# Kernel tuning notes

Measured on AMD Instinct MI355X. Metric: run time of the kernel, lower is better.

The kernel has to match this reference:

```python
import jax, jax.numpy as jnp
import numpy as np
import math

B = 8; T = 340; M = 32; H = 512; NH = 8; DH = H // NH; NB = 4; NA = 4
OBS = 64; MAXT = 1000
INFO = 3 * T; L = INFO + 2 * M  # 1084


def build_mask():
    # Replicates: causal tril over info tokens, then F.pad((0,M,M,0),0) and F.pad((M,0,0,M),1):
    # read-token columns (first M) visible to everyone; write-token rows (last M) attend to all;
    # read-token rows see only read tokens; info tokens are causal over info tokens.
    core = jnp.tril(jnp.ones((INFO, INFO), jnp.float32))
    m = jnp.zeros((L, L), jnp.float32)
    m = m.at[M:M + INFO, M:M + INFO].set(core)
    m = m.at[:, :M].set(1.0)
    m = m.at[-M:, :].set(1.0)
    return m


def layer_norm(x, g, b, eps=1e-5):
    mu = x.mean(-1, keepdims=True)
    var = ((x - mu) ** 2).mean(-1, keepdims=True)
    return (x - mu) / jnp.sqrt(var + eps) * g + b


def setup_inputs() -> dict:
    key = jax.random.key(0)
    ks = jax.random.split(key, 24)
    def n(k, shape, s=0.02):
        return jax.random.normal(k, shape, jnp.float32) * s
    return {
        "returns": jax.random.normal(ks[0], (B, T, 1), jnp.float32),
        "actions": jax.random.normal(ks[1], (B, T, 1), jnp.float32),
        "t_table": n(ks[2], (MAXT, H)),
        "s_table": n(ks[3], (OBS, H)),
        "Wr": n(ks[4], (H, 1)), "br": jnp.zeros((H,), jnp.float32),
        "Wa": n(ks[5], (H, 1)), "ba": jnp.zeros((H,), jnp.float32),
        "ln_e_g": jnp.ones((H,), jnp.float32), "ln_e_b": jnp.zeros((H,), jnp.float32),
        "read_mem": n(ks[6], (M, H)), "mem_tok": n(ks[7], (M, H)),
        "Wq": n(ks[8], (NB, H, H)), "bq": jnp.zeros((NB, H), jnp.float32),
        "Wk": n(ks[9], (NB, H, H)), "bk": jnp.zeros((NB, H), jnp.float32),
        "Wv": n(ks[10], (NB, H, H)), "bv": jnp.zeros((NB, H), jnp.float32),
        "Wo": n(ks[11], (NB, H, H)), "bo": jnp.zeros((NB, H), jnp.float32),
        "W1": n(ks[12], (NB, 4 * H, H)), "b1": jnp.zeros((NB, 4 * H), jnp.float32),
        "W2": n(ks[13], (NB, H, 4 * H)), "b2": jnp.zeros((NB, H), jnp.float32),
        "g1": jnp.ones((NB, H), jnp.float32), "be1": jnp.zeros((NB, H), jnp.float32),
        "g2": jnp.ones((NB, H), jnp.float32), "be2": jnp.zeros((NB, H), jnp.float32),
        "Wp": n(ks[14], (NA, H)), "bp": jnp.zeros((NA,), jnp.float32),
        "states": jax.random.randint(ks[15], (B, T), 0, OBS),
        "timestep": jax.random.randint(ks[16], (B, T), 0, MAXT),
    }


def _forward(returns, actions, t_table, s_table, Wr, br, Wa, ba, ln_e_g, ln_e_b,
             read_mem, mem_tok, Wq, bq, Wk, bk, Wv, bv, Wo, bo,
             W1, b1, W2, b2, g1, be1, g2, be2, Wp, bp, states, timestep):
    mask = build_mask()  # (L, L)
    te = t_table[timestep]                      # (B,T,H)
    re = returns @ Wr.T + br + te               # (B,T,H)
    se = s_table[states]                        # (B,T,H)
    ae = actions @ Wa.T + ba + te               # (B,T,H)
    hidden = jnp.stack([re, se, ae], axis=2).reshape(B, INFO, H)  # interleave r,s,a
    hidden = jnp.concatenate([
        jnp.broadcast_to(read_mem, (B, M, H)),
        hidden,
        jnp.broadcast_to(mem_tok, (B, M, H)),
    ], axis=1)                                  # (B,L,H)
    hidden = layer_norm(hidden, ln_e_g, ln_e_b)

    scale = 1.0 / math.sqrt(DH)

    def block(x, p):
        wq, bq_, wk, bk_, wv, bv_, wo, bo_, w1, b1_, w2, b2_, gg1, bb1, gg2, bb2 = p
        q = (x @ wq.T + bq_).reshape(B, L, NH, DH).transpose(0, 2, 1, 3)
        k = (x @ wk.T + bk_).reshape(B, L, NH, DH).transpose(0, 2, 1, 3)
        v = (x @ wv.T + bv_).reshape(B, L, NH, DH).transpose(0, 2, 1, 3)
        w = jnp.einsum('bnid,bnjd->bnij', q, k) * scale  # (B,NH,L,L)
        w = jnp.where(mask == 0, -jnp.inf, w)
        a = jax.nn.softmax(w, axis=-1)
        o = jnp.einsum('bnij,bnjd->bnid', a, v).transpose(0, 2, 1, 3).reshape(B, L, H)
        x = x + (o @ wo.T + bo_)
        x = layer_norm(x, gg1, bb1)
        m = jax.nn.gelu(x @ w1.T + b1_, approximate=False) @ w2.T + b2_
        x = layer_norm(x + m, gg2, bb2)
        return x, None

    hidden, _ = jax.lax.scan(
        block, hidden,
        (Wq, bq, Wk, bk, Wv, bv, Wo, bo, W1, b1, W2, b2, g1, be1, g2, be2))

    memory_output = hidden[:, -M:, :]
    core = hidden[:, M:-M, :].reshape(B, T, 3, H)
    action_logits = core[:, :, 1] @ Wp.T + bp   # predict from state-token hiddens
    return action_logits, memory_output


def reference(returns, actions, t_table, s_table, Wr, br, Wa, ba, ln_e_g, ln_e_b,
              read_mem, mem_tok, Wq, bq, Wk, bk, Wv, bv, Wo, bo,
              W1, b1, W2, b2, g1, be1, g2, be2, Wp, bp, states, timestep):
    return _forward(returns, actions, t_table, s_table, Wr, br, Wa, ba, ln_e_g, ln_e_b,
                    read_mem, mem_tok, Wq, bq, Wk, bk, Wv, bv, Wo, bo,
                    W1, b1, W2, b2, g1, be1, g2, be2, Wp, bp, states, timestep)
```

## Files before the change

### kernel.cpp

```cpp
#include <hip/hip_runtime.h>
#include <hip/hip_bf16.h>

typedef unsigned short ushort_t;
typedef __attribute__((ext_vector_type(8))) __bf16 bf16x8;
typedef __attribute__((ext_vector_type(4))) float f32x4;
typedef __attribute__((ext_vector_type(16))) float f32x16;
typedef __attribute__((ext_vector_type(2))) unsigned u32x2;
typedef __attribute__((ext_vector_type(4))) unsigned u32x4;

#define B_ 8
#define T_ 340
#define M_ 32
#define H_ 512
#define NH_ 8
#define DH_ 64
#define INFO_ 1020
#define L_ 1084
#define LP_ 1088
#define MROWS 8672
#define MPAD 8704
#define HMLP 2048

__device__ __forceinline__ ushort_t f2bf(float f) {
  unsigned u = __builtin_bit_cast(unsigned, f);
  unsigned r = (u + 0x7fffu + ((u >> 16) & 1u)) >> 16;
  return (ushort_t)r;
}

__device__ __forceinline__ float bflo(unsigned u) {
  return __builtin_bit_cast(float, u << 16);
}
__device__ __forceinline__ float bfhi(unsigned u) {
  return __builtin_bit_cast(float, u & 0xffff0000u);
}

__device__ __forceinline__ unsigned cvtpk_bf16(float lo, float hi) {
  unsigned r;
  asm volatile("v_cvt_pk_bf16_f32 %0, %1, %2" : "=v"(r) : "v"(lo), "v"(hi));
  return r;
}

__device__ __forceinline__ void gload16(const ushort_t* g, ushort_t* l) {
  __builtin_amdgcn_global_load_lds((const __attribute__((address_space(1))) unsigned*)g,
                                   (__attribute__((address_space(3))) unsigned*)l, 16, 0, 0);
}

__global__ __launch_bounds__(256) void zero_pads_kernel(ushort_t* Qb, ushort_t* Kb,
                                                        ushort_t* Vt, ushort_t* Ob) {
  int idx = blockIdx.x * 256 + threadIdx.x;
  if (idx < 16384) {
    int bh = idx >> 8;
    int rest = idx & 255;
    int l = L_ + (rest >> 6);
    int d = rest & 63;
    size_t o = ((size_t)bh * LP_ + l) * DH_ + d;
    Qb[o] = 0;
    Kb[o] = 0;
    Vt[((size_t)bh * DH_ + d) * LP_ + l] = 0;
  } else if (idx < 32768) {
    int j = idx - 16384;
    Ob[(size_t)MROWS * H_ + j] = 0;
  }
}

__global__ __launch_bounds__(256) void cvt8_kernel(const float* __restrict__ src,
                                                   ushort_t* __restrict__ dst, int n8) {
  int i = blockIdx.x * 256 + threadIdx.x;
  if (i >= n8) return;
  f32x4 a = ((const f32x4*)src)[2 * i];
  f32x4 b = ((const f32x4*)src)[2 * i + 1];
  u32x4 o;
  o.x = cvtpk_bf16(a[0], a[1]);
  o.y = cvtpk_bf16(a[2], a[3]);
  o.z = cvtpk_bf16(b[0], b[1]);
  o.w = cvtpk_bf16(b[2], b[3]);
  ((u32x4*)dst)[i] = o;
}

__global__ __launch_bounds__(256) void cvtqkv_kernel(const float* __restrict__ q,
                                                     const float* __restrict__ k,
                                                     const float* __restrict__ v,
                                                     ushort_t* __restrict__ dst) {
  int i8 = blockIdx.x * 256 + threadIdx.x;
  if (i8 >= 131072) return;
  int i = i8 * 8;
  int nb = i >> 18;
  int rem = i & 262143;
  size_t base8 = ((size_t)nb * 786432 + rem) >> 3;
  const float* srcs[3] = {q, k, v};
#pragma unroll
  for (int w = 0; w < 3; w++) {
    f32x4 a = ((const f32x4*)srcs[w])[2 * i8];
    f32x4 b = ((const f32x4*)srcs[w])[2 * i8 + 1];
    u32x4 o;
    o.x = cvtpk_bf16(a[0], a[1]);
    o.y = cvtpk_bf16(a[2], a[3]);
    o.z = cvtpk_bf16(b[0], b[1]);
    o.w = cvtpk_bf16(b[2], b[3]);
    ((u32x4*)dst)[base8 + (size_t)w * 32768] = o;
  }
}

__global__ __launch_bounds__(256) void biascat_kernel(const float* __restrict__ bq,
                                                      const float* __restrict__ bk,
                                                      const float* __restrict__ bv,
                                                      float* __restrict__ dst) {
  int i = blockIdx.x * 256 + threadIdx.x;
  if (i < 2048) {
    int nb = i >> 9, r = i & 511;
    float* d = dst + nb * 1536;
    d[r] = bq[i];
    d[512 + r] = bk[i];
    d[1024 + r] = bv[i];
  }
}

__global__ __launch_bounds__(256) void embed_ln_kernel(
    const float* __restrict__ returns, const float* __restrict__ actions,
    const float* __restrict__ t_table, const float* __restrict__ s_table,
    const float* __restrict__ Wr, const float* __restrict__ br,
    const float* __restrict__ Wa, const float* __restrict__ ba,
    const float* __restrict__ g, const float* __restrict__ be,
    const float* __restrict__ read_mem, const float* __restrict__ mem_tok,
    const int* __restrict__ states, const int* __restrict__ timestep,
    ushort_t* __restrict__ Xb) {
  const int row = blockIdx.x;
  const int tid = threadIdx.x;
  if (row >= MROWS) {
    Xb[(size_t)row * H_ + tid] = 0;
    Xb[(size_t)row * H_ + tid + 256] = 0;
    return;
  }
  const int b = row / L_, l = row - b * L_;
  float v[2];
#pragma unroll
  for (int s2 = 0; s2 < 2; s2++) {
    int hh = tid + s2 * 256;
    float val;
    if (l < M_) {
      val = read_mem[(size_t)l * H_ + hh];
    } else if (l >= M_ + INFO_) {
      val = mem_tok[(size_t)(l - M_ - INFO_) * H_ + hh];
    } else {
      int ii = l - M_;
      int t = ii / 3, c = ii - t * 3;
      int bt = b * T_ + t;
      if (c == 1) {
        val = s_table[(size_t)states[bt] * H_ + hh];
      } else {
        float te = t_table[(size_t)timestep[bt] * H_ + hh];
        val = (c == 0 ? returns[bt] * Wr[hh] + br[hh] : actions[bt] * Wa[hh] + ba[hh]) + te;
      }
    }
    v[s2] = val;
  }
  float sum = v[0] + v[1], sq = v[0] * v[0] + v[1] * v[1];
  __shared__ float sa[4], sb[4];
#pragma unroll
  for (int o = 1; o < 64; o <<= 1) {
    sum += __shfl_xor(sum, o);
    sq += __shfl_xor(sq, o);
  }
  int wv = tid >> 6, lane = tid & 63;
  if (lane == 0) { sa[wv] = sum; sb[wv] = sq; }
  __syncthreads();
  sum = sa[0] + sa[1] + sa[2] + sa[3];
  sq = sb[0] + sb[1] + sb[2] + sb[3];
  float mu = sum * (1.0f / H_);
  float var = sq * (1.0f / H_) - mu * mu;
  float rstd = rsqrtf(var + 1e-5f);
#pragma unroll
  for (int s2 = 0; s2 < 2; s2++) {
    int hh = tid + s2 * 256;
    float y = (v[s2] - mu) * rstd * g[hh] + be[hh];
    Xb[(size_t)row * H_ + hh] = f2bf(y);
  }
}

__global__ __launch_bounds__(256) void ln_add_kernel(ushort_t* __restrict__ Xb,
                                                     const ushort_t* __restrict__ Y,
                                                     const float* __restrict__ g,
                                                     const float* __restrict__ be) {
  const int row = blockIdx.x;
  const int tid = threadIdx.x;
  unsigned* xr = (unsigned*)(Xb + (size_t)row * H_);
  if (row >= MROWS) {
    xr[tid] = 0;
    return;
  }
  const unsigned* yr = (const unsigned*)(Y + (size_t)row * H_);
  unsigned xu = xr[tid], yu = yr[tid];
  float v0 = bflo(xu) + bflo(yu);
  float v1 = bfhi(xu) + bfhi(yu);
  float sum = v0 + v1, sq = v0 * v0 + v1 * v1;
  __shared__ float sa[4], sb[4];
#pragma unroll
  for (int o = 1; o < 64; o <<= 1) {
    sum += __shfl_xor(sum, o);
    sq += __shfl_xor(sq, o);
  }
  int wv = tid >> 6, lane = tid & 63;
  if (lane == 0) { sa[wv] = sum; sb[wv] = sq; }
  __syncthreads();
  sum = sa[0] + sa[1] + sa[2] + sa[3];
  sq = sb[0] + sb[1] + sb[2] + sb[3];
  float mu = sum * (1.0f / H_);
  float var = sq * (1.0f / H_) - mu * mu;
  float rstd = rsqrtf(var + 1e-5f);
  float g0 = g[2 * tid], g1v = g[2 * tid + 1];
  float b0 = be[2 * tid], b1v = be[2 * tid + 1];
  float n0 = (v0 - mu) * rstd * g0 + b0;
  float n1 = (v1 - mu) * rstd * g1v + b1v;
  xr[tid] = cvtpk_bf16(n0, n1);
}

template <int MODE>
__global__ __launch_bounds__(256, 3) void gemm_kernel(const ushort_t* __restrict__ A,
                                                      const ushort_t* __restrict__ W,
                                                      const float* __restrict__ bias,
                                                      void* __restrict__ o0,
                                                      void* __restrict__ o1,
                                                      void* __restrict__ o2, int Ntiles,
                                                      int K) {
  __shared__ ushort_t As[2][8192];
  __shared__ ushort_t Bs[2][4096];
  const int tid = threadIdx.x;
  const int job = (blockIdx.x & 7) * (gridDim.x >> 3) + (blockIdx.x >> 3);
  const int bx = job % Ntiles, by = job / Ntiles;
  const int m0 = by * 128, n0 = bx * 64;
  const int lane = tid & 63, wv = tid >> 6;
  const int wr = wv >> 1, wc = wv & 1;
  f32x4 acc[4][2] = {};

  const int srow = lane >> 3;
  const int kg = (lane & 7) ^ srow;
  const ushort_t* Asrc[4];
  const ushort_t* Bsrc[2];
#pragma unroll
  for (int g2 = 0; g2 < 4; g2++) {
    int row = wv * 32 + g2 * 8 + srow;
    Asrc[g2] = A + (size_t)(m0 + row) * K + kg * 8;
  }
#pragma unroll
  for (int g2 = 0; g2 < 2; g2++) {
    int row = wv * 16 + g2 * 8 + srow;
    Bsrc[g2] = W + (size_t)(n0 + row) * K + kg * 8;
  }
  ushort_t* ldsA[2] = {&As[0][wv * 2048], &As[1][wv * 2048]};
  ushort_t* ldsB[2] = {&Bs[0][wv * 1024], &Bs[1][wv * 1024]};

  const int NT = K >> 6;

#pragma unroll
  for (int g2 = 0; g2 < 4; g2++) gload16(Asrc[g2], ldsA[0] + g2 * 512);
#pragma unroll
  for (int g2 = 0; g2 < 2; g2++) gload16(Bsrc[g2], ldsB[0] + g2 * 512);

  const int q = lane >> 4, lr = lane & 15;
  const int s0 = q ^ (lr & 7);
  const int s1 = (4 + q) ^ (lr & 7);

  auto compute_tile = [&](int cur) {
    bf16x8 af[4][2], bfr[2][2];
#pragma unroll
    for (int mi = 0; mi < 4; mi++) {
      const ushort_t* rp = &As[cur][(wr * 64 + mi * 16 + lr) * 64];
      af[mi][0] = *(const bf16x8*)(rp + s0 * 8);
      af[mi][1] = *(const bf16x8*)(rp + s1 * 8);
    }
#pragma unroll
    for (int ni = 0; ni < 2; ni++) {
      const ushort_t* rp = &Bs[cur][(wc * 32 + ni * 16 + lr) * 64];
      bfr[ni][0] = *(const bf16x8*)(rp + s0 * 8);
      bfr[ni][1] = *(const bf16x8*)(rp + s1 * 8);
    }
#pragma unroll
    for (int kc = 0; kc < 2; kc++)
#pragma unroll
      for (int mi = 0; mi < 4; mi++)
#pragma unroll
        for (int ni = 0; ni < 2; ni++)
          acc[mi][ni] =
              __builtin_amdgcn_mfma_f32_16x16x32_bf16(af[mi][kc], bfr[ni][kc], acc[mi][ni], 0, 0, 0);
  };

  for (int kt = 0; kt < NT - 1; kt++) {
    const int cur = kt & 1, nxt = cur ^ 1;
    const int k0n = (kt + 1) << 6;
#pragma unroll
    for (int g2 = 0; g2 < 4; g2++) gload16(Asrc[g2] + k0n, ldsA[nxt] + g2 * 512);
#pragma unroll
    for (int g2 = 0; g2 < 2; g2++) gload16(Bsrc[g2] + k0n, ldsB[nxt] + g2 * 512);
    asm volatile("s_waitcnt vmcnt(6)" ::: "memory");
    __builtin_amdgcn_s_barrier();
    asm volatile("" ::: "memory");
    compute_tile(cur);
    asm volatile("" ::: "memory");
    __builtin_amdgcn_s_barrier();
  }
  {
    asm volatile("s_waitcnt vmcnt(0)" ::: "memory");
    __builtin_amdgcn_s_barrier();
    asm volatile("" ::: "memory");
    compute_tile((NT - 1) & 1);
  }

#pragma unroll
  for (int mi = 0; mi < 4; mi++) {
    const int mbase = m0 + wr * 64 + mi * 16 + ((lane >> 4) << 2);
    const bool mok = mbase < MROWS;
    int bb = 0, lbase = 0;
    if (MODE == 0) {
      bb = mbase / L_;
      lbase = mbase - bb * L_;
    }
#pragma unroll
    for (int ni = 0; ni < 2; ni++) {
      const int n = n0 + wc * 32 + ni * 16 + (lane & 15);
      float v[4];
#pragma unroll
      for (int r = 0; r < 4; r++) v[r] = acc[mi][ni][r] + bias[n];
      if (MODE == 0) {
        if (mok) {
          const int which = n >> 9, nn = n & 511;
          const int hh = nn >> 6, d = nn & 63;
          if (which == 0) {
            ushort_t* o = (ushort_t*)o0 + (((size_t)(bb * NH_ + hh)) * LP_ + lbase) * DH_ + d;
#pragma unroll
            for (int r = 0; r < 4; r++)
              o[(size_t)r * DH_] = f2bf(v[r] * 0.18033688011112043f);
          } else if (which == 1) {
            ushort_t* o = (ushort_t*)o1 + (((size_t)(bb * NH_ + hh)) * LP_ + lbase) * DH_ + d;
#pragma unroll
            for (int r = 0; r < 4; r++) o[(size_t)r * DH_] = f2bf(v[r]);
          } else {
            u32x2 w2;
            w2.x = cvtpk_bf16(v[0], v[1]);
            w2.y = cvtpk_bf16(v[2], v[3]);
            *(u32x2*)((ushort_t*)o2 + (((size_t)(bb * NH_ + hh)) * DH_ + d) * LP_ + lbase) = w2;
          }
        }
      } else if (MODE == 2) {
        if (mok) {
#pragma unroll
          for (int r = 0; r < 4; r++)
            ((ushort_t*)o0)[(size_t)(mbase + r) * H_ + n] = f2bf(v[r]);
        }
      } else {
#pragma unroll
        for (int r = 0; r < 4; r++) {
          float ge = 0.5f * v[r] * (1.0f + erff(v[r] * 0.70710678f));
          ((ushort_t*)o0)[(size_t)(mbase + r) * HMLP + n] = f2bf(ge);
        }
      }
    }
  }
}

__global__ __launch_bounds__(256, 3) void attn_kernel(const ushort_t* __restrict__ Qb,
                                                      const ushort_t* __restrict__ Kb,
                                                      const ushort_t* __restrict__ Vt,
                                                      ushort_t* __restrict__ Ob) {
  __shared__ ushort_t Klds[2][2048];
  __shared__ ushort_t Vlds[2][2048];
  const int tid = threadIdx.x;
  const int lane = tid & 63, wv = tid >> 6;
  const int xcd = blockIdx.x & 7, slot = blockIdx.x >> 3;
  const int g = slot >> 3, bhi = slot & 7;
  const int bh = (bhi << 3) | xcd;
  const int t = 33 - 4 * g - wv;
  const bool active = (t >= 0);
  const int b = bh >> 3, h = bh & 7;
  const int qb = t * 32;
  const int lq = lane & 31, hi = lane >> 5;
  const int nk_own = active ? ((t == 33) ? 34 : (t + 1)) : 0;
  const int nkmax = (g == 0) ? 34 : (34 - 4 * g);
  const int cmask = (t == 0) ? -1 : (nk_own - 1);
  const int i = qb + lq;

  const ushort_t* Qp = Qb + (size_t)bh * LP_ * DH_;
  const ushort_t* Kp = Kb + (size_t)bh * LP_ * DH_;
  const ushort_t* Vp = Vt + (size_t)bh * DH_ * LP_;

  const ushort_t* KsrcB =
      Kp + (size_t)(8 * wv + (lane >> 3)) * DH_ + (((lane & 7) ^ ((lane >> 3) & 7)) * 8);
  const ushort_t* VsrcB =
      Vp + (size_t)(16 * wv + (lane >> 2)) * LP_ + (((lane & 3) ^ ((lane >> 3) & 3)) * 8);
  ushort_t* KdstA = &Klds[0][wv * 512];
  ushort_t* KdstB = &Klds[1][wv * 512];
  ushort_t* VdstA = &Vlds[0][wv * 512];
  ushort_t* VdstB = &Vlds[1][wv * 512];

  bf16x8 qf[4];
  if (active) {
#pragma unroll
    for (int dc = 0; dc < 4; dc++)
      qf[dc] = *(const bf16x8*)(Qp + (size_t)(qb + lq) * DH_ + dc * 16 + hi * 8);
  }
  asm volatile("s_waitcnt vmcnt(0)" ::: "memory");

  f32x16 o0 = {}, o1 = {};
  float lsum = 0.f;

  int koff[4], voff[4];
#pragma unroll
  for (int dc = 0; dc < 4; dc++) koff[dc] = lq * 64 + (((dc * 2 + hi) ^ (lq & 7)) * 8);
#pragma unroll
  for (int f = 0; f < 4; f++) {
    int dt = f >> 1, cc = f & 1;
    voff[f] = (dt * 32 + lq) * 32 + ((((cc * 2 + hi) ^ ((lq >> 1) & 3))) * 8);
  }

  gload16(KsrcB, KdstA);
  gload16(VsrcB, VdstA);

  for (int c = 0; c < nkmax; c++) {
    const int cur = c & 1;
    const bool more = (c + 1 < nkmax);
    if (more) {
      const ushort_t* ks = KsrcB + (size_t)(c + 1) * 2048;
      const ushort_t* vs = VsrcB + (c + 1) * 32;
      if (cur) {
        gload16(ks, KdstA);
        gload16(vs, VdstA);
      } else {
        gload16(ks, KdstB);
        gload16(vs, VdstB);
      }
      asm volatile("s_waitcnt vmcnt(2)" ::: "memory");
    } else {
      asm volatile("s_waitcnt vmcnt(0)" ::: "memory");
    }
    __builtin_amdgcn_s_barrier();
    asm volatile("" ::: "memory");

    if (c < nk_own) {
      bf16x8 kf[4], vf[4];
#pragma unroll
      for (int dc = 0; dc < 4; dc++) kf[dc] = *(const bf16x8*)&Klds[cur][koff[dc]];
#pragma unroll
      for (int f = 0; f < 4; f++) vf[f] = *(const bf16x8*)&Vlds[cur][voff[f]];

      f32x16 s = {};
#pragma unroll
      for (int dc = 0; dc < 4; dc++)
        s = __builtin_amdgcn_mfma_f32_32x32x16_bf16(kf[dc], qf[dc], s, 0, 0, 0);
      float p[16];
      if (c == cmask) {
#pragma unroll
        for (int r = 0; r < 16; r++) {
          int jcol = c * 32 + (r & 3) + 8 * (r >> 2) + 4 * hi;
          bool ok = (jcol < L_) && ((jcol < M_) || (i >= M_ + INFO_) || (jcol <= i));
          p[r] = ok ? __builtin_amdgcn_exp2f(s[r]) : 0.f;
        }
      } else {
#pragma unroll
        for (int r = 0; r < 16; r++) p[r] = __builtin_amdgcn_exp2f(s[r]);
      }
      float u0 = (p[0] + p[1]) + (p[2] + p[3]);
      float u1 = (p[4] + p[5]) + (p[6] + p[7]);
      float u2 = (p[8] + p[9]) + (p[10] + p[11]);
      float u3 = (p[12] + p[13]) + (p[14] + p[15]);
      lsum += (u0 + u1) + (u2 + u3);
      bf16x8 pf[2];
#pragma unroll
      for (int cc = 0; cc < 2; cc++) {
        unsigned A01 = cvtpk_bf16(p[8 * cc + 0], p[8 * cc + 1]);
        unsigned A23 = cvtpk_bf16(p[8 * cc + 2], p[8 * cc + 3]);
        unsigned B45 = cvtpk_bf16(p[8 * cc + 4], p[8 * cc + 5]);
        unsigned B67 = cvtpk_bf16(p[8 * cc + 6], p[8 * cc + 7]);
        u32x2 r0 = __builtin_amdgcn_permlane32_swap(A01, B45, false, false);
        u32x2 r1 = __builtin_amdgcn_permlane32_swap(A23, B67, false, false);
        u32x4 w = {r0.x, r1.x, r0.y, r1.y};
        pf[cc] = __builtin_bit_cast(bf16x8, w);
      }
      o0 = __builtin_amdgcn_mfma_f32_32x32x16_bf16(vf[0], pf[0], o0, 0, 0, 0);
      o0 = __builtin_amdgcn_mfma_f32_32x32x16_bf16(vf[1], pf[1], o0, 0, 0, 0);
      o1 = __builtin_amdgcn_mfma_f32_32x32x16_bf16(vf[2], pf[0], o1, 0, 0, 0);
      o1 = __builtin_amdgcn_mfma_f32_32x32x16_bf16(vf[3], pf[1], o1, 0, 0, 0);
    }
    asm volatile("" ::: "memory");
    __builtin_amdgcn_s_barrier();
  }

  if (active) {
    u32x2 tt = __builtin_amdgcn_permlane32_swap(__builtin_bit_cast(unsigned, lsum),
                                                __builtin_bit_cast(unsigned, lsum), false, false);
    lsum = __builtin_bit_cast(float, tt.x) + __builtin_bit_cast(float, tt.y);
    if (i < L_) {
      const float inv = 1.0f / lsum;
      ushort_t* orow = Ob + ((size_t)(b * L_ + i)) * H_ + h * DH_;
#pragma unroll
      for (int dt = 0; dt < 2; dt++) {
#pragma unroll
        for (int q2 = 0; q2 < 4; q2++) {
          float v0 = (dt ? o1[4 * q2 + 0] : o0[4 * q2 + 0]) * inv;
          float v1 = (dt ? o1[4 * q2 + 1] : o0[4 * q2 + 1]) * inv;
          float v2 = (dt ? o1[4 * q2 + 2] : o0[4 * q2 + 2]) * inv;
          float v3 = (dt ? o1[4 * q2 + 3] : o0[4 * q2 + 3]) * inv;
          int dbase = dt * 32 + 8 * q2 + 4 * hi;
          *(unsigned*)(orow + dbase) = cvtpk_bf16(v0, v1);
          *(unsigned*)(orow + dbase + 2) = cvtpk_bf16(v2, v3);
        }
      }
    }
  }
}

__global__ __launch_bounds__(64) void logits_kernel(const ushort_t* __restrict__ Xb,
                                                    const float* __restrict__ Wp,
                                                    const float* __restrict__ bp,
                                                    float* __restrict__ out) {
  const int bt = blockIdx.x;
  const int b = bt / T_, t = bt - b * T_;
  const int lane = threadIdx.x;
  const ushort_t* xr = Xb + ((size_t)(b * L_ + M_ + 3 * t + 1)) * H_ + lane * 8;
  u32x4 xv = *(const u32x4*)xr;
  float x0[8];
#pragma unroll
  for (int ii = 0; ii < 4; ii++) {
    unsigned u = xv[ii];
    x0[2 * ii] = bflo(u);
    x0[2 * ii + 1] = bfhi(u);
  }
#pragma unroll
  for (int a = 0; a < 4; a++) {
    const float* wr2 = Wp + (size_t)a * H_ + lane * 8;
    float p = 0.f;
#pragma unroll
    for (int ii = 0; ii < 8; ii++) p += x0[ii] * wr2[ii];
#pragma unroll
    for (int o = 1; o < 64; o <<= 1) p += __shfl_xor(p, o);
    if (lane == 0) out[(size_t)bt * 4 + a] = p + bp[a];
  }
}

__global__ __launch_bounds__(256) void memout_kernel(const ushort_t* __restrict__ Xb,
                                                     float* __restrict__ out) {
  int idx = blockIdx.x * 256 + threadIdx.x;
  if (idx < B_ * M_ * H_ / 2) {
    int e = idx * 2;
    int b = e >> 14;
    int rest = e & 16383;
    int r = rest >> 9;
    int hh = rest & 511;
    unsigned u = *(const unsigned*)&Xb[((size_t)(b * L_ + M_ + INFO_ + r)) * H_ + hh];
    out[e] = bflo(u);
    out[e + 1] = bfhi(u);
  }
}

extern "C" void kernel_launch(void* const* d_in, const int* in_sizes, int n_in, void* d_out,
                              int out_size, void* d_ws, size_t ws_size, hipStream_t stream) {
  const float* returns = (const float*)d_in[0];
  const float* actions = (const float*)d_in[1];
  const float* t_table = (const float*)d_in[2];
  const float* s_table = (const float*)d_in[3];
  const float* Wr = (const float*)d_in[4];
  const float* br = (const float*)d_in[5];
  const float* Wa = (const float*)d_in[6];
  const float* ba = (const float*)d_in[7];
  const float* ln_e_g = (const float*)d_in[8];
  const float* ln_e_b = (const float*)d_in[9];
  const float* read_mem = (const float*)d_in[10];
  const float* mem_tok = (const float*)d_in[11];
  const float* Wq = (const float*)d_in[12];
  const float* bq = (const float*)d_in[13];
  const float* Wk = (const float*)d_in[14];
  const float* bk = (const float*)d_in[15];
  const float* Wv = (const float*)d_in[16];
  const float* bv = (const float*)d_in[17];
  const float* Wo = (const float*)d_in[18];
  const float* bo = (const float*)d_in[19];
  const float* W1 = (const float*)d_in[20];
  const float* b1 = (const float*)d_in[21];
  const float* W2 = (const float*)d_in[22];
  const float* b2 = (const float*)d_in[23];
  const float* g1 = (const float*)d_in[24];
  const float* be1 = (const float*)d_in[25];
  const float* g2 = (const float*)d_in[26];
  const float* be2 = (const float*)d_in[27];
  const float* Wp = (const float*)d_in[28];
  const float* bp = (const float*)d_in[29];
  const int* states = (const int*)d_in[30];
  const int* timestep = (const int*)d_in[31];

  char* ws = (char*)d_ws;
  size_t off = 0;
  auto alloc = [&](size_t bytes) -> char* {
    char* p = ws + off;
    off += (bytes + 255) & ~(size_t)255;
    return p;
  };
  ushort_t* Xb = (ushort_t*)alloc((size_t)MPAD * H_ * 2);
  ushort_t* Y = (ushort_t*)alloc((size_t)MPAD * H_ * 2);
  ushort_t* Qb = (ushort_t*)alloc((size_t)B_ * NH_ * LP_ * DH_ * 2);
  ushort_t* Kb2 = (ushort_t*)alloc((size_t)B_ * NH_ * LP_ * DH_ * 2);
  ushort_t* Vt = (ushort_t*)alloc((size_t)B_ * NH_ * DH_ * LP_ * 2);
  ushort_t* Ob = (ushort_t*)alloc((size_t)MPAD * H_ * 2);
  ushort_t* Hm = (ushort_t*)alloc((size_t)MPAD * HMLP * 2);
  ushort_t* Wqkvb = (ushort_t*)alloc((size_t)4 * 1536 * 512 * 2);
  ushort_t* Wob = (ushort_t*)alloc((size_t)4 * 512 * 512 * 2);
  ushort_t* W1b = (ushort_t*)alloc((size_t)4 * 2048 * 512 * 2);
  ushort_t* W2b = (ushort_t*)alloc((size_t)4 * 512 * 2048 * 2);
  float* biascat = (float*)alloc((size_t)4 * 1536 * 4);

  zero_pads_kernel<<<128, 256, 0, stream>>>(Qb, Kb2, Vt, Ob);
  cvtqkv_kernel<<<512, 256, 0, stream>>>(Wq, Wk, Wv, Wqkvb);
  biascat_kernel<<<8, 256, 0, stream>>>(bq, bk, bv, biascat);
  cvt8_kernel<<<512, 256, 0, stream>>>(Wo, Wob, 4 * 512 * 512 / 8);
  cvt8_kernel<<<2048, 256, 0, stream>>>(W1, W1b, 4 * 2048 * 512 / 8);
  cvt8_kernel<<<2048, 256, 0, stream>>>(W2, W2b, 4 * 512 * 2048 / 8);

  embed_ln_kernel<<<MPAD, 256, 0, stream>>>(returns, actions, t_table, s_table, Wr, br, Wa,
                                            ba, ln_e_g, ln_e_b, read_mem, mem_tok, states,
                                            timestep, Xb);

  for (int nb = 0; nb < 4; ++nb) {
    const size_t wo512 = (size_t)nb * 512 * 512;
    const size_t woqkv = (size_t)nb * 1536 * 512;
    const size_t wo1 = (size_t)nb * 2048 * 512;
    gemm_kernel<0><<<68 * 24, 256, 0, stream>>>(Xb, Wqkvb + woqkv, biascat + nb * 1536, Qb,
                                                Kb2, Vt, 24, 512);
    attn_kernel<<<576, 256, 0, stream>>>(Qb, Kb2, Vt, Ob);
    gemm_kernel<2><<<68 * 8, 256, 0, stream>>>(Ob, Wob + wo512, bo + nb * 512, Y, nullptr,
                                               nullptr, 8, 512);
    ln_add_kernel<<<MPAD, 256, 0, stream>>>(Xb, Y, g1 + nb * 512, be1 + nb * 512);
    gemm_kernel<3><<<68 * 32, 256, 0, stream>>>(Xb, W1b + wo1, b1 + nb * 2048, Hm, nullptr,
                                                nullptr, 32, 512);
    gemm_kernel<2><<<68 * 8, 256, 0, stream>>>(Hm, W2b + wo1, b2 + nb * 512, Y, nullptr,
                                               nullptr, 8, 2048);
    ln_add_kernel<<<MPAD, 256, 0, stream>>>(Xb, Y, g2 + nb * 512, be2 + nb * 512);
  }

  logits_kernel<<<B_ * T_, 64, 0, stream>>>(Xb, Wp, bp, (float*)d_out);
  memout_kernel<<<256, 256, 0, stream>>>(Xb, (float*)d_out + (size_t)B_ * T_ * 4);
}
```

Measured before the change: 627.0 us.

## Triple-buffer LDS prefetch in GEMM and attention kernels

Both the GEMM and attention kernels move from double to triple buffering, issuing global-to-LDS loads two tiles ahead and adjusting vmcnt waits to match. The aim is to hide more global memory latency behind MFMA compute. In exchange the GEMM's LDS use grows from 48KB to 72KB and its launch bound drops from 3 to 2 blocks per CU, lowering occupancy. The attention kernel also drops the wait on the Q loads, so that wait now folds into the first loop iteration's vmcnt.

New measurement: 804.3 us. +28.3%, slower.

```diff
diff --git a/kernel.cpp b/kernel.cpp
--- a/kernel.cpp
+++ b/kernel.cpp
@@ -215,15 +215,15 @@
 }
 
 template <int MODE>
-__global__ __launch_bounds__(256, 3) void gemm_kernel(const ushort_t* __restrict__ A,
+__global__ __launch_bounds__(256, 2) void gemm_kernel(const ushort_t* __restrict__ A,
                                                       const ushort_t* __restrict__ W,
                                                       const float* __restrict__ bias,
                                                       void* __restrict__ o0,
                                                       void* __restrict__ o1,
                                                       void* __restrict__ o2, int Ntiles,
                                                       int K) {
-  __shared__ ushort_t As[2][8192];
-  __shared__ ushort_t Bs[2][4096];
+  __shared__ ushort_t As[3][8192];
+  __shared__ ushort_t Bs[3][4096];
   const int tid = threadIdx.x;
   const int job = (blockIdx.x & 7) * (gridDim.x >> 3) + (blockIdx.x >> 3);
   const int bx = job % Ntiles, by = job / Ntiles;
@@ -246,15 +246,21 @@
     int row = wv * 16 + g2 * 8 + srow;
     Bsrc[g2] = W + (size_t)(n0 + row) * K + kg * 8;
   }
-  ushort_t* ldsA[2] = {&As[0][wv * 2048], &As[1][wv * 2048]};
-  ushort_t* ldsB[2] = {&Bs[0][wv * 1024], &Bs[1][wv * 1024]};
 
   const int NT = K >> 6;
 
-#pragma unroll
-  for (int g2 = 0; g2 < 4; g2++) gload16(Asrc[g2], ldsA[0] + g2 * 512);
-#pragma unroll
-  for (int g2 = 0; g2 < 2; g2++) gload16(Bsrc[g2], ldsB[0] + g2 * 512);
+  auto stage = [&](int kt, int buf) {
+    const int k0 = kt << 6;
+    ushort_t* la = &As[buf][wv * 2048];
+    ushort_t* lb = &Bs[buf][wv * 1024];
+#pragma unroll
+    for (int g2 = 0; g2 < 4; g2++) gload16(Asrc[g2] + k0, la + g2 * 512);
+#pragma unroll
+    for (int g2 = 0; g2 < 2; g2++) gload16(Bsrc[g2] + k0, lb + g2 * 512);
+  };
+
+  stage(0, 0);
+  if (NT > 1) stage(1, 1);
 
   const int q = lane >> 4, lr = lane & 15;
   const int s0 = q ^ (lr & 7);
@@ -284,25 +290,21 @@
               __builtin_amdgcn_mfma_f32_16x16x32_bf16(af[mi][kc], bfr[ni][kc], acc[mi][ni], 0, 0, 0);
   };
 
-  for (int kt = 0; kt < NT - 1; kt++) {
-    const int cur = kt & 1, nxt = cur ^ 1;
-    const int k0n = (kt + 1) << 6;
-#pragma unroll
-    for (int g2 = 0; g2 < 4; g2++) gload16(Asrc[g2] + k0n, ldsA[nxt] + g2 * 512);
-#pragma unroll
-    for (int g2 = 0; g2 < 2; g2++) gload16(Bsrc[g2] + k0n, ldsB[nxt] + g2 * 512);
-    asm volatile("s_waitcnt vmcnt(6)" ::: "memory");
+  for (int kt = 0; kt < NT; kt++) {
+    const int nxt2 = kt + 2;
+    if (nxt2 < NT) stage(nxt2, nxt2 % 3);
+    if (nxt2 < NT) {
+      asm volatile("s_waitcnt vmcnt(12)" ::: "memory");
+    } else if (kt + 1 < NT) {
+      asm volatile("s_waitcnt vmcnt(6)" ::: "memory");
+    } else {
+      asm volatile("s_waitcnt vmcnt(0)" ::: "memory");
+    }
     __builtin_amdgcn_s_barrier();
     asm volatile("" ::: "memory");
-    compute_tile(cur);
+    compute_tile(kt % 3);
     asm volatile("" ::: "memory");
     __builtin_amdgcn_s_barrier();
-  }
-  {
-    asm volatile("s_waitcnt vmcnt(0)" ::: "memory");
-    __builtin_amdgcn_s_barrier();
-    asm volatile("" ::: "memory");
-    compute_tile((NT - 1) & 1);
   }
 
 #pragma unroll
@@ -361,8 +363,8 @@
                                                       const ushort_t* __restrict__ Kb,
                                                       const ushort_t* __restrict__ Vt,
                                                       ushort_t* __restrict__ Ob) {
-  __shared__ ushort_t Klds[2][2048];
-  __shared__ ushort_t Vlds[2][2048];
+  __shared__ ushort_t Klds[3][2048];
+  __shared__ ushort_t Vlds[3][2048];
   const int tid = threadIdx.x;
   const int lane = tid & 63, wv = tid >> 6;
   const int xcd = blockIdx.x & 7, slot = blockIdx.x >> 3;
@@ -386,10 +388,14 @@
       Kp + (size_t)(8 * wv + (lane >> 3)) * DH_ + (((lane & 7) ^ ((lane >> 3) & 7)) * 8);
   const ushort_t* VsrcB =
       Vp + (size_t)(16 * wv + (lane >> 2)) * LP_ + (((lane & 3) ^ ((lane >> 3) & 3)) * 8);
-  ushort_t* KdstA = &Klds[0][wv * 512];
-  ushort_t* KdstB = &Klds[1][wv * 512];
-  ushort_t* VdstA = &Vlds[0][wv * 512];
-  ushort_t* VdstB = &Vlds[1][wv * 512];
+
+  auto stageKV = [&](int c, int buf) {
+    gload16(KsrcB + (size_t)c * 2048, &Klds[buf][wv * 512]);
+    gload16(VsrcB + c * 32, &Vlds[buf][wv * 512]);
+  };
+
+  stageKV(0, 0);
+  if (nkmax > 1) stageKV(1, 1);
 
   bf16x8 qf[4];
   if (active) {
@@ -397,7 +403,6 @@
     for (int dc = 0; dc < 4; dc++)
       qf[dc] = *(const bf16x8*)(Qp + (size_t)(qb + lq) * DH_ + dc * 16 + hi * 8);
   }
-  asm volatile("s_waitcnt vmcnt(0)" ::: "memory");
 
   f32x16 o0 = {}, o1 = {};
   float lsum = 0.f;
@@ -411,22 +416,13 @@
     voff[f] = (dt * 32 + lq) * 32 + ((((cc * 2 + hi) ^ ((lq >> 1) & 3))) * 8);
   }
 
-  gload16(KsrcB, KdstA);
-  gload16(VsrcB, VdstA);
-
   for (int c = 0; c < nkmax; c++) {
-    const int cur = c & 1;
-    const bool more = (c + 1 < nkmax);
-    if (more) {
-      const ushort_t* ks = KsrcB + (size_t)(c + 1) * 2048;
-      const ushort_t* vs = VsrcB + (c + 1) * 32;
-      if (cur) {
-        gload16(ks, KdstA);
-        gload16(vs, VdstA);
-      } else {
-        gload16(ks, KdstB);
-        gload16(vs, VdstB);
-      }
+    const int cur = c % 3;
+    const int n2 = c + 2;
+    if (n2 < nkmax) stageKV(n2, n2 % 3);
+    if (n2 < nkmax) {
+      asm volatile("s_waitcnt vmcnt(4)" ::: "memory");
+    } else if (c + 1 < nkmax) {
       asm volatile("s_waitcnt vmcnt(2)" ::: "memory");
     } else {
       asm volatile("s_waitcnt vmcnt(0)" ::: "memory");
```
